# Kernel tuning notes

Hardware: AMD Instinct MI355X
Metric: run time of the kernel (lower is better)

Reference implementation:

```python
import jax, jax.numpy as jnp
import numpy as np

B, S, D = 4, 4096, 768
E, SLOTS = 16, 1  # n_experts, slots_per_expert
H = 4 * D


def setup_inputs() -> dict:
    key = jax.random.key(0)
    k = jax.random.split(key, 6)
    scale1 = 1.0 / np.sqrt(D)
    scale2 = 1.0 / np.sqrt(H)
    return {
        "x": jax.random.normal(k[0], (B, S, D), dtype=jnp.float32),
        "phi": jax.random.normal(k[1], (D, E * SLOTS), dtype=jnp.float32),
        "W1": jax.random.normal(k[2], (E, D, H), dtype=jnp.float32) * scale1,
        "b1": jnp.zeros((E, H), dtype=jnp.float32),
        "W2": jax.random.normal(k[3], (E, H, D), dtype=jnp.float32) * scale2,
        "b2": jnp.zeros((E, D), dtype=jnp.float32),
    }


def reference(x, phi, W1, b1, W2, b2):
    # logits: [B, S, E*SLOTS]
    logits = jnp.einsum("bsd,dn->bsn", x, phi)
    dispatch_weights = jax.nn.softmax(logits, axis=-1)  # over slots
    combine_weights = jax.nn.softmax(logits, axis=1)    # over sequence
    # xs: [B, E*SLOTS, D] = dispatch^T @ x
    xs = jnp.einsum("bsn,bsd->bnd", dispatch_weights, x)
    xs = xs.reshape(B, E, SLOTS, D)
    # per-expert FFN, batched over experts: GELU (exact, as torch nn.GELU default)
    h = jnp.einsum("bepd,edh->beph", xs, W1) + b1[None, :, None, :]
    h = jax.nn.gelu(h, approximate=False)
    ys = jnp.einsum("beph,ehd->bepd", h, W2) + b2[None, :, None, :]
    ys = ys.reshape(B, E * SLOTS, D)
    # combine: [B, S, D]
    y = jnp.einsum("bsn,bnd->bsd", combine_weights, ys)
    return y
```

## Files before the change

kernel.cpp:

```cpp
#include <hip/hip_runtime.h>
#include <math.h>

constexpr int B = 4, S = 4096, D = 768, E = 16, N = 16, H = 3072;
constexpr int SCH = 32;
constexpr int NSCH = S / SCH;
constexpr int HL = 96;
constexpr int NHC = H / HL;
constexpr int LBLK = 32;
constexpr int LPB = S / LBLK;

constexpr size_t OFF_LOG  = 0;
constexpr size_t OFF_DW   = OFF_LOG + (size_t)B * S * N;
constexpr size_t OFF_PCM  = OFF_DW + (size_t)B * S * N;
constexpr size_t OFF_PCS  = OFF_PCM + (size_t)B * LPB * N;
constexpr size_t OFF_CMAX = OFF_PCS + (size_t)B * LPB * N;
constexpr size_t OFF_CSUM = OFF_CMAX + (size_t)B * N;
constexpr size_t OFF_XSP  = OFF_CSUM + (size_t)B * N;
constexpr size_t OFF_XS   = OFF_XSP + (size_t)B * NSCH * N * D;
constexpr size_t OFF_YSP  = OFF_XS + (size_t)B * N * D;
constexpr size_t OFF_YS   = OFF_YSP + (size_t)NHC * B * E * D;

__global__ __launch_bounds__(256) void k_logits(const float* __restrict__ x,
                                                const float* __restrict__ phi,
                                                float* __restrict__ logits,
                                                float* __restrict__ dw,
                                                float* __restrict__ pcm,
                                                float* __restrict__ pcs) {
    __shared__ float ph[16][D];
    __shared__ float rm[16][16], rs[16][16];
    const int t = threadIdx.x;
    const int blk = blockIdx.x;
    const int b = blk / LPB;
    const int s0 = (blk % LPB) * LBLK;

#pragma unroll
    for (int i = 0; i < 12; ++i) {
        const int idx = i * 1024 + t * 4;
        const float4 v = *reinterpret_cast<const float4*>(phi + idx);
        const int d0 = idx >> 4;
        const int n0 = idx & 15;
        ph[n0 + 0][d0] = v.x;
        ph[n0 + 1][d0] = v.y;
        ph[n0 + 2][d0] = v.z;
        ph[n0 + 3][d0] = v.w;
    }
    __syncthreads();

    const int gid = t >> 4;
    const int ln = t & 15;
    const int s = s0 + gid * 2;
    const float* xr0 = x + ((size_t)b * S + s) * D;
    const float* xr1 = xr0 + D;

    float4 a0[12], a1[12];
#pragma unroll
    for (int j = 0; j < 12; ++j) {
        a0[j] = *reinterpret_cast<const float4*>(xr0 + j * 64 + ln * 4);
        a1[j] = *reinterpret_cast<const float4*>(xr1 + j * 64 + ln * 4);
    }
    float p0[16], p1[16];
#pragma unroll
    for (int n = 0; n < 16; ++n) {
        float q0 = 0.f, q1 = 0.f;
#pragma unroll
        for (int j = 0; j < 12; ++j) {
            const float4 pv = *reinterpret_cast<const float4*>(&ph[n][j * 64 + ln * 4]);
            q0 = fmaf(a0[j].x, pv.x, q0); q1 = fmaf(a1[j].x, pv.x, q1);
            q0 = fmaf(a0[j].y, pv.y, q0); q1 = fmaf(a1[j].y, pv.y, q1);
            q0 = fmaf(a0[j].z, pv.z, q0); q1 = fmaf(a1[j].z, pv.z, q1);
            q0 = fmaf(a0[j].w, pv.w, q0); q1 = fmaf(a1[j].w, pv.w, q1);
        }
        p0[n] = q0; p1[n] = q1;
    }
#pragma unroll
    for (int m = 1; m < 16; m <<= 1) {
#pragma unroll
        for (int n = 0; n < 16; ++n) {
            p0[n] += __shfl_xor(p0[n], m, 64);
            p1[n] += __shfl_xor(p1[n], m, 64);
        }
    }
    float m0 = -1e30f, m1 = -1e30f;
#pragma unroll
    for (int n = 0; n < 16; ++n) { m0 = fmaxf(m0, p0[n]); m1 = fmaxf(m1, p1[n]); }
    float su0 = 0.f, su1 = 0.f;
#pragma unroll
    for (int n = 0; n < 16; ++n) { su0 += __expf(p0[n] - m0); su1 += __expf(p1[n] - m1); }
    const size_t o0 = ((size_t)b * S + s) * N + ln;
    logits[o0] = p0[ln];
    logits[o0 + N] = p1[ln];
    dw[o0] = __expf(p0[ln] - m0) / su0;
    dw[o0 + N] = __expf(p1[ln] - m1) / su1;

    const float mm = fmaxf(p0[ln], p1[ln]);
    const float ss = __expf(p0[ln] - mm) + __expf(p1[ln] - mm);
    rm[gid][ln] = mm;
    rs[gid][ln] = ss;
    __syncthreads();
    if (t < 16) {
        float M = -1e30f;
#pragma unroll
        for (int g = 0; g < 16; ++g) M = fmaxf(M, rm[g][t]);
        float SS = 0.f;
#pragma unroll
        for (int g = 0; g < 16; ++g) SS += rs[g][t] * __expf(rm[g][t] - M);
        pcm[blk * 16 + t] = M;
        pcs[blk * 16 + t] = SS;
    }
}

__global__ __launch_bounds__(192) void k_xsp(const float* __restrict__ x,
                                             const float* __restrict__ dw,
                                             float* __restrict__ xsp) {
    const int blk = blockIdx.x;
    const int b = blk / NSCH;
    const int c = blk % NSCH;
    const int t = threadIdx.x;
    const int d = t * 4;
    float4 a[16];
#pragma unroll
    for (int n = 0; n < 16; ++n) a[n] = float4{0.f, 0.f, 0.f, 0.f};
    const float* xb = x + ((size_t)b * S + (size_t)c * SCH) * D + d;
    const float* dwb = dw + ((size_t)b * S + (size_t)c * SCH) * N;
#pragma unroll 2
    for (int s = 0; s < SCH; ++s) {
        const float4 xv = *reinterpret_cast<const float4*>(xb + (size_t)s * D);
#pragma unroll
        for (int n = 0; n < 16; ++n) {
            const float w = dwb[s * N + n];
            a[n].x = fmaf(w, xv.x, a[n].x);
            a[n].y = fmaf(w, xv.y, a[n].y);
            a[n].z = fmaf(w, xv.z, a[n].z);
            a[n].w = fmaf(w, xv.w, a[n].w);
        }
    }
    float* o = xsp + (size_t)blk * N * D + d;
#pragma unroll
    for (int n = 0; n < 16; ++n)
        *reinterpret_cast<float4*>(o + (size_t)n * D) = a[n];
}

__global__ __launch_bounds__(256) void k_xsred_cmerge(const float* __restrict__ xsp,
                                                      float* __restrict__ xs,
                                                      const float* __restrict__ pcm,
                                                      const float* __restrict__ pcs,
                                                      float* __restrict__ cmax,
                                                      float* __restrict__ csum) {
    const int t = threadIdx.x;
    if (blockIdx.x < 192) {
        const int i = blockIdx.x * 256 + t;
        const int b = i / (N * D);
        const int rem = i % (N * D);
        const float* p = xsp + (size_t)b * NSCH * N * D + rem;
        float sum = 0.f;
#pragma unroll 4
        for (int c = 0; c < NSCH; ++c) sum += p[(size_t)c * N * D];
        xs[i] = sum;
    } else if (t < 64) {
        const int b = t >> 4, n = t & 15;
        float M = -1e30f;
#pragma unroll 8
        for (int c = 0; c < LPB; ++c) M = fmaxf(M, pcm[((size_t)b * LPB + c) * 16 + n]);
        float SS = 0.f;
#pragma unroll 8
        for (int c = 0; c < LPB; ++c)
            SS += pcs[((size_t)b * LPB + c) * 16 + n] * __expf(pcm[((size_t)b * LPB + c) * 16 + n] - M);
        cmax[b * 16 + n] = M;
        csum[b * 16 + n] = SS;
    }
}

__global__ __launch_bounds__(384) void k_ffn(const float* __restrict__ xs,
                                             const float* __restrict__ W1,
                                             const float* __restrict__ b1,
                                             const float* __restrict__ W2,
                                             float* __restrict__ ysp) {
    __shared__ float xs_lds[D][4];
    __shared__ float4 red_lds[16][HL];
    __shared__ float4 yq_lds[2][192][4];
    __shared__ float4 h_lds[HL];

    const int t = threadIdx.x;
    const int e = blockIdx.x / NHC;
    const int hc = blockIdx.x % NHC;

    for (int idx = t; idx < D; idx += 384) {
#pragma unroll
        for (int b = 0; b < 4; ++b)
            xs_lds[idx][b] = xs[((size_t)b * N + e) * D + idx];
    }
    __syncthreads();

    {
        const int c4 = (t % 24) * 4;
        const int q = t / 24;
        float4 h0{0,0,0,0}, h1{0,0,0,0}, h2{0,0,0,0}, h3{0,0,0,0};
        const float* w1p = W1 + ((size_t)e * D + (size_t)q * 48) * H + hc * HL + c4;
#pragma unroll 8
        for (int dd = 0; dd < 48; ++dd) {
            const float4 w = *reinterpret_cast<const float4*>(w1p + (size_t)dd * H);
            const float* xv = &xs_lds[q * 48 + dd][0];
            const float x0 = xv[0], x1 = xv[1], x2 = xv[2], x3 = xv[3];
            h0.x = fmaf(x0, w.x, h0.x); h0.y = fmaf(x0, w.y, h0.y);
            h0.z = fmaf(x0, w.z, h0.z); h0.w = fmaf(x0, w.w, h0.w);
            h1.x = fmaf(x1, w.x, h1.x); h1.y = fmaf(x1, w.y, h1.y);
            h1.z = fmaf(x1, w.z, h1.z); h1.w = fmaf(x1, w.w, h1.w);
            h2.x = fmaf(x2, w.x, h2.x); h2.y = fmaf(x2, w.y, h2.y);
            h2.z = fmaf(x2, w.z, h2.z); h2.w = fmaf(x2, w.w, h2.w);
            h3.x = fmaf(x3, w.x, h3.x); h3.y = fmaf(x3, w.y, h3.y);
            h3.z = fmaf(x3, w.z, h3.z); h3.w = fmaf(x3, w.w, h3.w);
        }
        red_lds[q][c4 + 0] = float4{h0.x, h1.x, h2.x, h3.x};
        red_lds[q][c4 + 1] = float4{h0.y, h1.y, h2.y, h3.y};
        red_lds[q][c4 + 2] = float4{h0.z, h1.z, h2.z, h3.z};
        red_lds[q][c4 + 3] = float4{h0.w, h1.w, h2.w, h3.w};
    }
    __syncthreads();
    if (t < HL) {
        float4 s{0,0,0,0};
#pragma unroll
        for (int q = 0; q < 16; ++q) {
            const float4 v = red_lds[q][t];
            s.x += v.x; s.y += v.y; s.z += v.z; s.w += v.w;
        }
        const float bias = b1[(size_t)e * H + hc * HL + t];
        s.x += bias; s.y += bias; s.z += bias; s.w += bias;
        s.x = 0.5f * s.x * (1.0f + erff(s.x * 0.70710678118654752f));
        s.y = 0.5f * s.y * (1.0f + erff(s.y * 0.70710678118654752f));
        s.z = 0.5f * s.z * (1.0f + erff(s.z * 0.70710678118654752f));
        s.w = 0.5f * s.w * (1.0f + erff(s.w * 0.70710678118654752f));
        h_lds[t] = s;
    }
    __syncthreads();

    {
        const int dgrp = t % 192;
        const int d4 = dgrp * 4;
        const int kq = t / 192;
        float4 y0{0,0,0,0}, y1{0,0,0,0}, y2{0,0,0,0}, y3{0,0,0,0};
        const float* w2p = W2 + ((size_t)e * H + hc * HL + kq * 48) * D + d4;
#pragma unroll 8
        for (int kk = 0; kk < 48; ++kk) {
            const float4 w = *reinterpret_cast<const float4*>(w2p + (size_t)kk * D);
            const float4 hv = h_lds[kq * 48 + kk];
            y0.x = fmaf(hv.x, w.x, y0.x); y0.y = fmaf(hv.x, w.y, y0.y);
            y0.z = fmaf(hv.x, w.z, y0.z); y0.w = fmaf(hv.x, w.w, y0.w);
            y1.x = fmaf(hv.y, w.x, y1.x); y1.y = fmaf(hv.y, w.y, y1.y);
            y1.z = fmaf(hv.y, w.z, y1.z); y1.w = fmaf(hv.y, w.w, y1.w);
            y2.x = fmaf(hv.z, w.x, y2.x); y2.y = fmaf(hv.z, w.y, y2.y);
            y2.z = fmaf(hv.z, w.z, y2.z); y2.w = fmaf(hv.z, w.w, y2.w);
            y3.x = fmaf(hv.w, w.x, y3.x); y3.y = fmaf(hv.w, w.y, y3.y);
            y3.z = fmaf(hv.w, w.z, y3.z); y3.w = fmaf(hv.w, w.w, y3.w);
        }
        yq_lds[kq][dgrp][0] = y0;
        yq_lds[kq][dgrp][1] = y1;
        yq_lds[kq][dgrp][2] = y2;
        yq_lds[kq][dgrp][3] = y3;
    }
    __syncthreads();
    if (t < 192) {
        const int d4 = t * 4;
#pragma unroll
        for (int b = 0; b < 4; ++b) {
            const float4 u = yq_lds[0][t][b];
            const float4 v = yq_lds[1][t][b];
            float4 r{u.x + v.x, u.y + v.y, u.z + v.z, u.w + v.w};
            *reinterpret_cast<float4*>(ysp + (((size_t)hc * B + b) * E + e) * D + d4) = r;
        }
    }
}

__global__ __launch_bounds__(256) void k_ysred(const float* __restrict__ ysp,
                                               const float* __restrict__ b2,
                                               float* __restrict__ ys) {
    const int i4 = blockIdx.x * 256 + threadIdx.x;
    const int rem4 = i4 % (E * D / 4);
    float4 v = *reinterpret_cast<const float4*>(b2 + (size_t)rem4 * 4);
#pragma unroll 8
    for (int p = 0; p < NHC; ++p) {
        const float4 u = *reinterpret_cast<const float4*>(ysp + (size_t)p * B * E * D + (size_t)i4 * 4);
        v.x += u.x; v.y += u.y; v.z += u.z; v.w += u.w;
    }
    *reinterpret_cast<float4*>(ys + (size_t)i4 * 4) = v;
}

__global__ __launch_bounds__(192) void k_combine(const float* __restrict__ logits,
                                                 const float* __restrict__ cmax,
                                                 const float* __restrict__ csum,
                                                 const float* __restrict__ ys,
                                                 float* __restrict__ y) {
    const int blk = blockIdx.x;
    const int b = blk / (S / 8);
    const int s0 = (blk % (S / 8)) * 8;
    const int t = threadIdx.x;
    const int d4 = t * 4;

    float4 ysr[16];
    float cm[16], ci[16];
#pragma unroll
    for (int n = 0; n < 16; ++n) {
        ysr[n] = *reinterpret_cast<const float4*>(ys + ((size_t)b * N + n) * D + d4);
        cm[n] = cmax[b * N + n];
        ci[n] = 1.0f / csum[b * N + n];
    }
#pragma unroll
    for (int r = 0; r < 8; ++r) {
        const int s = s0 + r;
        const float* lrow = logits + ((size_t)b * S + s) * N;
        float4 acc{0,0,0,0};
#pragma unroll
        for (int n = 0; n < 16; ++n) {
            const float cw = __expf(lrow[n] - cm[n]) * ci[n];
            acc.x = fmaf(cw, ysr[n].x, acc.x);
            acc.y = fmaf(cw, ysr[n].y, acc.y);
            acc.z = fmaf(cw, ysr[n].z, acc.z);
            acc.w = fmaf(cw, ysr[n].w, acc.w);
        }
        *reinterpret_cast<float4*>(y + ((size_t)b * S + s) * D + d4) = acc;
    }
}

extern "C" void kernel_launch(void* const* d_in, const int* in_sizes, int n_in,
                              void* d_out, int out_size, void* d_ws, size_t ws_size,
                              hipStream_t stream) {
    const float* x   = (const float*)d_in[0];
    const float* phi = (const float*)d_in[1];
    const float* W1  = (const float*)d_in[2];
    const float* b1  = (const float*)d_in[3];
    const float* W2  = (const float*)d_in[4];
    const float* b2  = (const float*)d_in[5];
    float* y = (float*)d_out;
    float* ws = (float*)d_ws;

    float* logits = ws + OFF_LOG;
    float* dw     = ws + OFF_DW;
    float* pcm    = ws + OFF_PCM;
    float* pcs    = ws + OFF_PCS;
    float* cmax   = ws + OFF_CMAX;
    float* csum   = ws + OFF_CSUM;
    float* xsp    = ws + OFF_XSP;
    float* xs     = ws + OFF_XS;
    float* ysp    = ws + OFF_YSP;
    float* ys     = ws + OFF_YS;

    k_logits<<<B * LPB, 256, 0, stream>>>(x, phi, logits, dw, pcm, pcs);
    k_xsp<<<B * NSCH, 192, 0, stream>>>(x, dw, xsp);
    k_xsred_cmerge<<<193, 256, 0, stream>>>(xsp, xs, pcm, pcs, cmax, csum);
    k_ffn<<<E * NHC, 384, 0, stream>>>(xs, W1, b1, W2, ysp);
    k_ysred<<<48, 256, 0, stream>>>(ysp, b2, ys);
    k_combine<<<B * (S / 8), 192, 0, stream>>>(logits, cmax, csum, ys, y);
}
```

Before: 152.9 us.

## Split fused expert FFN into separate W1, GELU-reduce and W2 kernels

The single fused FFN kernel, which split work over hidden-dimension chunks and reduced inside the block, is replaced by three kernels. The first splits the W1 product over 24-row slices of D and reads full contiguous H rows. A second kernel reduces the partial products, adds the bias and applies GELU. A third runs the W2 product over 96-row hidden chunks. The aim is more coalesced, streaming weight reads and a simpler per-block inner loop; the cost is a large partial-sum buffer (32 slices of B*E*H floats) written and read back, plus an extra launch.

After: 171.2 us. +11.9%, slower.

```diff
diff --git a/kernel.cpp b/kernel.cpp
--- a/kernel.cpp
+++ b/kernel.cpp
@@ -4,8 +4,10 @@
 constexpr int B = 4, S = 4096, D = 768, E = 16, N = 16, H = 3072;
 constexpr int SCH = 32;
 constexpr int NSCH = S / SCH;
-constexpr int HL = 96;
-constexpr int NHC = H / HL;
+constexpr int DL = 24;
+constexpr int NDC = D / DL;
+constexpr int HL2 = 96;
+constexpr int NHC2 = H / HL2;
 constexpr int LBLK = 32;
 constexpr int LPB = S / LBLK;
 
@@ -17,8 +19,17 @@
 constexpr size_t OFF_CSUM = OFF_CMAX + (size_t)B * N;
 constexpr size_t OFF_XSP  = OFF_CSUM + (size_t)B * N;
 constexpr size_t OFF_XS   = OFF_XSP + (size_t)B * NSCH * N * D;
-constexpr size_t OFF_YSP  = OFF_XS + (size_t)B * N * D;
-constexpr size_t OFF_YS   = OFF_YSP + (size_t)NHC * B * E * D;
+constexpr size_t OFF_HP   = OFF_XS + (size_t)B * N * D;
+constexpr size_t OFF_HACT = OFF_HP + (size_t)NDC * B * E * H;
+constexpr size_t OFF_YSP  = OFF_HACT + (size_t)B * E * H;
+constexpr size_t OFF_YS   = OFF_YSP + (size_t)NHC2 * B * E * D;
+
+__device__ __forceinline__ void fma4(float4& a, float s, const float4& w) {
+    a.x = fmaf(s, w.x, a.x);
+    a.y = fmaf(s, w.y, a.y);
+    a.z = fmaf(s, w.z, a.z);
+    a.w = fmaf(s, w.w, a.w);
+}
 
 __global__ __launch_bounds__(256) void k_logits(const float* __restrict__ x,
                                                 const float* __restrict__ phi,
@@ -170,104 +181,100 @@
     }
 }
 
-__global__ __launch_bounds__(384) void k_ffn(const float* __restrict__ xs,
-                                             const float* __restrict__ W1,
-                                             const float* __restrict__ b1,
-                                             const float* __restrict__ W2,
-                                             float* __restrict__ ysp) {
-    __shared__ float xs_lds[D][4];
-    __shared__ float4 red_lds[16][HL];
-    __shared__ float4 yq_lds[2][192][4];
-    __shared__ float4 h_lds[HL];
-
-    const int t = threadIdx.x;
-    const int e = blockIdx.x / NHC;
-    const int hc = blockIdx.x % NHC;
-
-    for (int idx = t; idx < D; idx += 384) {
+__global__ __launch_bounds__(256) void k_ffn1(const float* __restrict__ xs,
+                                              const float* __restrict__ W1,
+                                              float* __restrict__ hp) {
+    __shared__ __align__(16) float xs_lds[DL][4];
+    const int t = threadIdx.x;
+    const int e = blockIdx.x / NDC;
+    const int dc = blockIdx.x % NDC;
+    const int d0 = dc * DL;
+    if (t < DL * 4) {
+        const int dd = t >> 2, b = t & 3;
+        xs_lds[dd][b] = xs[((size_t)b * N + e) * D + d0 + dd];
+    }
+    __syncthreads();
+
+    float4 acc[3][4];
+#pragma unroll
+    for (int k = 0; k < 3; ++k)
+#pragma unroll
+        for (int b = 0; b < 4; ++b) acc[k][b] = float4{0.f, 0.f, 0.f, 0.f};
+
+    const float* wbase = W1 + ((size_t)e * D + d0) * H + t * 4;
+#pragma unroll 4
+    for (int dd = 0; dd < DL; ++dd) {
+        const float4 xv = *reinterpret_cast<const float4*>(&xs_lds[dd][0]);
+        const float* wrow = wbase + (size_t)dd * H;
+        float4 w[3];
+        w[0] = *reinterpret_cast<const float4*>(wrow);
+        w[1] = *reinterpret_cast<const float4*>(wrow + 1024);
+        w[2] = *reinterpret_cast<const float4*>(wrow + 2048);
+#pragma unroll
+        for (int k = 0; k < 3; ++k) {
+            fma4(acc[k][0], xv.x, w[k]);
+            fma4(acc[k][1], xv.y, w[k]);
+            fma4(acc[k][2], xv.z, w[k]);
+            fma4(acc[k][3], xv.w, w[k]);
+        }
+    }
+#pragma unroll
+    for (int k = 0; k < 3; ++k)
 #pragma unroll
         for (int b = 0; b < 4; ++b)
-            xs_lds[idx][b] = xs[((size_t)b * N + e) * D + idx];
+            *reinterpret_cast<float4*>(hp + (((size_t)dc * 4 + b) * E + e) * H + k * 1024 + t * 4) = acc[k][b];
+}
+
+__global__ __launch_bounds__(256) void k_gelu(const float* __restrict__ hp,
+                                              const float* __restrict__ b1,
+                                              float* __restrict__ hact) {
+    const int i4 = blockIdx.x * 256 + threadIdx.x;
+    const int rem4 = i4 % (E * H / 4);
+    float4 v = *reinterpret_cast<const float4*>(b1 + (size_t)rem4 * 4);
+#pragma unroll 8
+    for (int dc = 0; dc < NDC; ++dc) {
+        const float4 p = *reinterpret_cast<const float4*>(hp + (size_t)dc * B * E * H + (size_t)i4 * 4);
+        v.x += p.x; v.y += p.y; v.z += p.z; v.w += p.w;
+    }
+    float4 g;
+    g.x = 0.5f * v.x * (1.0f + erff(v.x * 0.70710678118654752f));
+    g.y = 0.5f * v.y * (1.0f + erff(v.y * 0.70710678118654752f));
+    g.z = 0.5f * v.z * (1.0f + erff(v.z * 0.70710678118654752f));
+    g.w = 0.5f * v.w * (1.0f + erff(v.w * 0.70710678118654752f));
+    *reinterpret_cast<float4*>(hact + (size_t)i4 * 4) = g;
+}
+
+__global__ __launch_bounds__(192) void k_ffn2(const float* __restrict__ hact,
+                                              const float* __restrict__ W2,
+                                              float* __restrict__ ysp) {
+    __shared__ __align__(16) float h_lds[HL2][4];
+    const int t = threadIdx.x;
+    const int e = blockIdx.x / NHC2;
+    const int hc = blockIdx.x % NHC2;
+    const int h0 = hc * HL2;
+    for (int idx = t; idx < HL2 * 4; idx += 192) {
+        const int hh = idx >> 2, b = idx & 3;
+        h_lds[hh][b] = hact[((size_t)b * E + e) * H + h0 + hh];
     }
     __syncthreads();
 
-    {
-        const int c4 = (t % 24) * 4;
-        const int q = t / 24;
-        float4 h0{0,0,0,0}, h1{0,0,0,0}, h2{0,0,0,0}, h3{0,0,0,0};
-        const float* w1p = W1 + ((size_t)e * D + (size_t)q * 48) * H + hc * HL + c4;
-#pragma unroll 8
-        for (int dd = 0; dd < 48; ++dd) {
-            const float4 w = *reinterpret_cast<const float4*>(w1p + (size_t)dd * H);
-            const float* xv = &xs_lds[q * 48 + dd][0];
-            const float x0 = xv[0], x1 = xv[1], x2 = xv[2], x3 = xv[3];
-            h0.x = fmaf(x0, w.x, h0.x); h0.y = fmaf(x0, w.y, h0.y);
-            h0.z = fmaf(x0, w.z, h0.z); h0.w = fmaf(x0, w.w, h0.w);
-            h1.x = fmaf(x1, w.x, h1.x); h1.y = fmaf(x1, w.y, h1.y);
-            h1.z = fmaf(x1, w.z, h1.z); h1.w = fmaf(x1, w.w, h1.w);
-            h2.x = fmaf(x2, w.x, h2.x); h2.y = fmaf(x2, w.y, h2.y);
-            h2.z = fmaf(x2, w.z, h2.z); h2.w = fmaf(x2, w.w, h2.w);
-            h3.x = fmaf(x3, w.x, h3.x); h3.y = fmaf(x3, w.y, h3.y);
-            h3.z = fmaf(x3, w.z, h3.z); h3.w = fmaf(x3, w.w, h3.w);
-        }
-        red_lds[q][c4 + 0] = float4{h0.x, h1.x, h2.x, h3.x};
-        red_lds[q][c4 + 1] = float4{h0.y, h1.y, h2.y, h3.y};
-        red_lds[q][c4 + 2] = float4{h0.z, h1.z, h2.z, h3.z};
-        red_lds[q][c4 + 3] = float4{h0.w, h1.w, h2.w, h3.w};
-    }
-    __syncthreads();
-    if (t < HL) {
-        float4 s{0,0,0,0};
-#pragma unroll
-        for (int q = 0; q < 16; ++q) {
-            const float4 v = red_lds[q][t];
-            s.x += v.x; s.y += v.y; s.z += v.z; s.w += v.w;
-        }
-        const float bias = b1[(size_t)e * H + hc * HL + t];
-        s.x += bias; s.y += bias; s.z += bias; s.w += bias;
-        s.x = 0.5f * s.x * (1.0f + erff(s.x * 0.70710678118654752f));
-        s.y = 0.5f * s.y * (1.0f + erff(s.y * 0.70710678118654752f));
-        s.z = 0.5f * s.z * (1.0f + erff(s.z * 0.70710678118654752f));
-        s.w = 0.5f * s.w * (1.0f + erff(s.w * 0.70710678118654752f));
-        h_lds[t] = s;
-    }
-    __syncthreads();
-
-    {
-        const int dgrp = t % 192;
-        const int d4 = dgrp * 4;
-        const int kq = t / 192;
-        float4 y0{0,0,0,0}, y1{0,0,0,0}, y2{0,0,0,0}, y3{0,0,0,0};
-        const float* w2p = W2 + ((size_t)e * H + hc * HL + kq * 48) * D + d4;
-#pragma unroll 8
-        for (int kk = 0; kk < 48; ++kk) {
-            const float4 w = *reinterpret_cast<const float4*>(w2p + (size_t)kk * D);
-            const float4 hv = h_lds[kq * 48 + kk];
-            y0.x = fmaf(hv.x, w.x, y0.x); y0.y = fmaf(hv.x, w.y, y0.y);
-            y0.z = fmaf(hv.x, w.z, y0.z); y0.w = fmaf(hv.x, w.w, y0.w);
-            y1.x = fmaf(hv.y, w.x, y1.x); y1.y = fmaf(hv.y, w.y, y1.y);
-            y1.z = fmaf(hv.y, w.z, y1.z); y1.w = fmaf(hv.y, w.w, y1.w);
-            y2.x = fmaf(hv.z, w.x, y2.x); y2.y = fmaf(hv.z, w.y, y2.y);
-            y2.z = fmaf(hv.z, w.z, y2.z); y2.w = fmaf(hv.z, w.w, y2.w);
-            y3.x = fmaf(hv.w, w.x, y3.x); y3.y = fmaf(hv.w, w.y, y3.y);
-            y3.z = fmaf(hv.w, w.z, y3.z); y3.w = fmaf(hv.w, w.w, y3.w);
-        }
-        yq_lds[kq][dgrp][0] = y0;
-        yq_lds[kq][dgrp][1] = y1;
-        yq_lds[kq][dgrp][2] = y2;
-        yq_lds[kq][dgrp][3] = y3;
-    }
-    __syncthreads();
-    if (t < 192) {
-        const int d4 = t * 4;
-#pragma unroll
-        for (int b = 0; b < 4; ++b) {
-            const float4 u = yq_lds[0][t][b];
-            const float4 v = yq_lds[1][t][b];
-            float4 r{u.x + v.x, u.y + v.y, u.z + v.z, u.w + v.w};
-            *reinterpret_cast<float4*>(ysp + (((size_t)hc * B + b) * E + e) * D + d4) = r;
-        }
-    }
+    float4 acc[4];
+#pragma unroll
+    for (int b = 0; b < 4; ++b) acc[b] = float4{0.f, 0.f, 0.f, 0.f};
+
+    const float* wbase = W2 + ((size_t)e * H + h0) * D + t * 4;
+#pragma unroll 8
+    for (int kk = 0; kk < HL2; ++kk) {
+        const float4 hv = *reinterpret_cast<const float4*>(&h_lds[kk][0]);
+        const float4 w = *reinterpret_cast<const float4*>(wbase + (size_t)kk * D);
+        fma4(acc[0], hv.x, w);
+        fma4(acc[1], hv.y, w);
+        fma4(acc[2], hv.z, w);
+        fma4(acc[3], hv.w, w);
+    }
+#pragma unroll
+    for (int b = 0; b < 4; ++b)
+        *reinterpret_cast<float4*>(ysp + (((size_t)hc * 4 + b) * E + e) * D + t * 4) = acc[b];
 }
 
 __global__ __launch_bounds__(256) void k_ysred(const float* __restrict__ ysp,
@@ -277,8 +284,8 @@
     const int rem4 = i4 % (E * D / 4);
     float4 v = *reinterpret_cast<const float4*>(b2 + (size_t)rem4 * 4);
 #pragma unroll 8
-    for (int p = 0; p < NHC; ++p) {
-        const float4 u = *reinterpret_cast<const float4*>(ysp + (size_t)p * B * E * D + (size_t)i4 * 4);
+    for (int hc = 0; hc < NHC2; ++hc) {
+        const float4 u = *reinterpret_cast<const float4*>(ysp + (size_t)hc * B * E * D + (size_t)i4 * 4);
         v.x += u.x; v.y += u.y; v.z += u.z; v.w += u.w;
     }
     *reinterpret_cast<float4*>(ys + (size_t)i4 * 4) = v;
@@ -307,7 +314,7 @@
     for (int r = 0; r < 8; ++r) {
         const int s = s0 + r;
         const float* lrow = logits + ((size_t)b * S + s) * N;
-        float4 acc{0,0,0,0};
+        float4 acc{0, 0, 0, 0};
 #pragma unroll
         for (int n = 0; n < 16; ++n) {
             const float cw = __expf(lrow[n] - cm[n]) * ci[n];
@@ -340,13 +347,17 @@
     float* csum   = ws + OFF_CSUM;
     float* xsp    = ws + OFF_XSP;
     float* xs     = ws + OFF_XS;
+    float* hp     = ws + OFF_HP;
+    float* hact   = ws + OFF_HACT;
     float* ysp    = ws + OFF_YSP;
     float* ys     = ws + OFF_YS;
 
     k_logits<<<B * LPB, 256, 0, stream>>>(x, phi, logits, dw, pcm, pcs);
     k_xsp<<<B * NSCH, 192, 0, stream>>>(x, dw, xsp);
     k_xsred_cmerge<<<193, 256, 0, stream>>>(xsp, xs, pcm, pcs, cmax, csum);
-    k_ffn<<<E * NHC, 384, 0, stream>>>(xs, W1, b1, W2, ysp);
-    k_ysred<<<48, 256, 0, stream>>>(ysp, b2, ys);
+    k_ffn1<<<E * NDC, 256, 0, stream>>>(xs, W1, hp);
+    k_gelu<<<(B * E * H / 4) / 256, 256, 0, stream>>>(hp, b1, hact);
+    k_ffn2<<<E * NHC2, 192, 0, stream>>>(hact, W2, ysp);
+    k_ysred<<<(B * E * D / 4) / 256, 256, 0, stream>>>(ysp, b2, ys);
     k_combine<<<B * (S / 8), 192, 0, stream>>>(logits, cmax, csum, ys, y);
 }
```
